# Kernel optimization log

Measured on AMD Instinct MI355X. Metric: run time of the kernel, lower is better.

Reference implementation:

```python
import jax, jax.numpy as jnp
import numpy as np
from jax import lax

GRID_SIZE = 5
SPLINE_ORDER = 3
N_COEF = GRID_SIZE + SPLINE_ORDER  # 8 b-spline basis functions per input
GRID_LO, GRID_HI = -1.0, 1.0


def _grid():
    h = (GRID_HI - GRID_LO) / GRID_SIZE
    return jnp.arange(-SPLINE_ORDER, GRID_SIZE + SPLINE_ORDER + 1, dtype=jnp.float32) * h + GRID_LO


def _bsplines(x):
    # x: [..., in] -> [..., in, N_COEF] via Cox-de Boor recursion (efficient-kan)
    grid = _grid()
    x = x[..., None]
    bases = ((x >= grid[:-1]) & (x < grid[1:])).astype(x.dtype)
    for j in range(1, SPLINE_ORDER + 1):
        bases = ((x - grid[:-(j + 1)]) / (grid[j:-1] - grid[:-(j + 1)]) * bases[..., :-1]
                 + (grid[j + 1:] - x) / (grid[j + 1:] - grid[1:-j]) * bases[..., 1:])
    return bases


def _kan_linear(x, base_w, spline_w):
    # x: [..., in]; base_w: [out, in]; spline_w: [out, in, N_COEF]
    base = jax.nn.silu(x) @ base_w.T
    b = _bsplines(x).reshape(x.shape[:-1] + (-1,))  # [..., in*N_COEF]
    return base + b @ spline_w.reshape(spline_w.shape[0], -1).T


def _kan_conv(x, base_w, spline_w):
    # x: [B, C, H, W]; 3x3 valid KAN convolution
    patches = lax.conv_general_dilated_patches(x, (3, 3), (1, 1), 'VALID')  # [B, C*9, H-2, W-2]
    p = patches.transpose(0, 2, 3, 1)  # [B, Ho, Wo, C*9]
    out = _kan_linear(p, base_w, spline_w)  # [B, Ho, Wo, out]
    return out.transpose(0, 3, 1, 2)


def _maxpool2(x):
    return lax.reduce_window(x, -jnp.inf, lax.max, (1, 1, 2, 2), (1, 1, 2, 2), 'VALID')


def setup_inputs() -> dict:
    key = jax.random.key(0)
    ks = jax.random.split(key, 12)
    B = 2048
    x = jax.random.uniform(ks[0], (B, 1, 28, 28), dtype=jnp.float32)
    s = 0.1
    return {
        'x': x,
        'bw1': jax.random.normal(ks[1], (5, 9), dtype=jnp.float32) * s,
        'sw1': jax.random.normal(ks[2], (5, 9, N_COEF), dtype=jnp.float32) * s,
        'bw2': jax.random.normal(ks[3], (5, 45), dtype=jnp.float32) * s,
        'sw2': jax.random.normal(ks[4], (5, 45, N_COEF), dtype=jnp.float32) * s,
        'bw3': jax.random.normal(ks[5], (2, 45), dtype=jnp.float32) * s,
        'sw3': jax.random.normal(ks[6], (2, 45, N_COEF), dtype=jnp.float32) * s,
        'w1': jax.random.normal(ks[7], (500, 162), dtype=jnp.float32) * 0.05,
        'b1': jnp.zeros((500,), dtype=jnp.float32),
        'w2': jax.random.normal(ks[8], (10, 500), dtype=jnp.float32) * 0.05,
        'b2': jnp.zeros((10,), dtype=jnp.float32),
    }


def reference(x, bw1, sw1, bw2, sw2, bw3, sw3, w1, b1, w2, b2):
    h = _kan_conv(x, bw1, sw1)       # [B, 5, 26, 26]
    h = _maxpool2(h)                 # [B, 5, 13, 13]
    h = _kan_conv(h, bw2, sw2)       # [B, 5, 11, 11]
    h = _kan_conv(h, bw3, sw3)       # [B, 2, 9, 9]
    h = h.reshape(h.shape[0], -1)    # [B, 162]
    h = jax.nn.relu(h @ w1.T + b1)   # [B, 500]
    return h @ w2.T + b2             # [B, 10]
```

## Files before the change

### kernel.cpp

```cpp
#include <hip/hip_runtime.h>


typedef _Float16 h2 __attribute__((ext_vector_type(2)));

__device__ __forceinline__ h2 u2h(unsigned int u) {
  union { unsigned int x; h2 h; } v; v.x = u; return v.h;
}
__device__ __forceinline__ unsigned short f2h_bits(float x) {
  union { _Float16 h; unsigned short u; } v; v.h = (_Float16)x; return v.u;
}
__device__ __forceinline__ unsigned int pack2h(float a, float b) {
  return (unsigned int)f2h_bits(a) | ((unsigned int)f2h_bits(b) << 16);
}
__device__ __forceinline__ float fdot2(h2 a, h2 b, float c) {
  return __builtin_amdgcn_fdot2(a, b, c, false);
}

__device__ __forceinline__ void featurize_regs(float v, uint4& bs, float& silu) {
  silu = v / (1.0f + __expf(-v));
  bs.x = 0u; bs.y = 0u; bs.z = 0u; bs.w = 0u;
  float u = fmaf(v, 2.5f, 5.5f);
  if (u >= 0.0f && u < 11.0f) {
    float tf = floorf(u);
    float f = u - tf, f2 = f * f, f3 = f2 * f, om = 1.0f - f;
    const float c6 = 1.0f / 6.0f;
    float w0 = om * om * om * c6;
    float w1 = (3.0f * f3 - 6.0f * f2 + 4.0f) * c6;
    float w2 = (-3.0f * f3 + 3.0f * f2 + 3.0f * f + 1.0f) * c6;
    float w3 = f3 * c6;
    unsigned long long w01 =
        (unsigned long long)f2h_bits(w0) |
        ((unsigned long long)f2h_bits(w1) << 16) |
        ((unsigned long long)f2h_bits(w2) << 32) |
        ((unsigned long long)f2h_bits(w3) << 48);
    int t = (int)tf;
    int s = 16 * t - 48;
    unsigned long long lo, hi;
    if (s >= 0) {
      lo = (s < 64) ? (w01 << s) : 0ull;
      hi = (s == 0) ? 0ull : ((s < 64) ? (w01 >> (64 - s)) : (w01 << (s - 64)));
    } else {
      lo = w01 >> (-s);
      hi = 0ull;
    }
    bs.x = (unsigned int)lo; bs.y = (unsigned int)(lo >> 32);
    bs.z = (unsigned int)hi; bs.w = (unsigned int)(hi >> 32);
  }
}

__global__ __launch_bounds__(256) void k_prep(
    const float* __restrict__ bw1, const float* __restrict__ sw1,
    const float* __restrict__ bw2, const float* __restrict__ sw2,
    const float* __restrict__ bw3, const float* __restrict__ sw3,
    const float* __restrict__ w1, const float* __restrict__ w2,
    unsigned int* __restrict__ V1s, float* __restrict__ V1b,
    unsigned int* __restrict__ V2s, float* __restrict__ V2b,
    unsigned int* __restrict__ V3s, float* __restrict__ V3b,
    unsigned int* __restrict__ W1p4, float* __restrict__ W2p) {
  int t = blockIdx.x * 256 + threadIdx.x;
  if (t < 180) {
    int p = t & 3, o = (t >> 2) % 5, in = t / 20;
    V1s[t] = pack2h(sw1[(o * 9 + in) * 8 + 2 * p], sw1[(o * 9 + in) * 8 + 2 * p + 1]);
  }
  if (t < 45)  { int o = t % 5, in = t / 5; V1b[t] = bw1[o * 9 + in]; }
  if (t < 900) {
    int p = t & 3, o = (t >> 2) % 5, in = t / 20;
    V2s[t] = pack2h(sw2[(o * 45 + in) * 8 + 2 * p], sw2[(o * 45 + in) * 8 + 2 * p + 1]);
  }
  if (t < 225) { int o = t % 5, in = t / 5; V2b[t] = bw2[o * 45 + in]; }
  if (t < 360) {
    int p = t & 3, o = (t >> 2) & 1, in = t / 8;
    V3s[t] = pack2h(sw3[(o * 45 + in) * 8 + 2 * p], sw3[(o * 45 + in) * 8 + 2 * p + 1]);
  }
  if (t < 90)  { int o = t % 2, in = t / 2; V3b[t] = bw3[o * 45 + in]; }
  if (t < 43008) {
    int j = t & 3, o = (t >> 2) & 511, kpq = t >> 11;
    int kp = kpq * 4 + j;
    W1p4[t] = (o < 500 && kp < 81)
                  ? pack2h(w1[o * 162 + 2 * kp], w1[o * 162 + 2 * kp + 1])
                  : 0u;
  }
  if (t < 5120) {
    int o = t >> 9, k = t & 511;
    W2p[t] = (k < 500) ? w2[o * 500 + k] : 0.0f;
  }
}

__global__ __launch_bounds__(64, 2) void k_fused(
    const float* __restrict__ x,
    const unsigned int* __restrict__ V1s, const float* __restrict__ V1b,
    const unsigned int* __restrict__ V2s, const float* __restrict__ V2b,
    const unsigned int* __restrict__ V3s, const float* __restrict__ V3b,
    const unsigned int* __restrict__ W1p4, const float* __restrict__ W2p,
    const float* __restrict__ b1, const float* __restrict__ b2,
    float* __restrict__ out) {
  __shared__ uint4 bas[845];
  __shared__ float slu[845];
  float*        basF = (float*)bas;
  unsigned int* hpk  = (unsigned int*)slu + 256;
  const int b = blockIdx.x;
  const int lane = threadIdx.x;

  for (int l = lane; l < 784; l += 64) {
    uint4 bs; float sl;
    featurize_regs(x[b * 784 + l], bs, sl);
    bas[l] = bs; slu[l] = sl;
  }

  float h1v[3][5];
  #pragma unroll 1
  for (int it = 0; it < 3; ++it) {
    int p = it * 64 + lane;
    if (p < 169) {
      int py = p / 13, px = p % 13;
      int r0 = py * 2, c0 = px * 2;
      float wacc[4][5];
      #pragma unroll
      for (int wi = 0; wi < 4; ++wi)
        #pragma unroll
        for (int o = 0; o < 5; ++o) wacc[wi][o] = 0.0f;
      #pragma unroll
      for (int r = 0; r < 4; ++r) {
        uint4 q[4]; float sl[4];
        #pragma unroll
        for (int c = 0; c < 4; ++c) {
          q[c]  = bas[(r0 + r) * 28 + c0 + c];
          sl[c] = slu[(r0 + r) * 28 + c0 + c];
        }
        #pragma unroll
        for (int c = 0; c < 4; ++c) {
          h2 a0 = u2h(q[c].x), a1 = u2h(q[c].y), a2 = u2h(q[c].z), a3 = u2h(q[c].w);
          #pragma unroll
          for (int dy = 0; dy < 2; ++dy) {
            #pragma unroll
            for (int dx = 0; dx < 2; ++dx) {
              int ky = r - dy, kx = c - dx;
              if (ky >= 0 && ky < 3 && kx >= 0 && kx < 3) {
                const unsigned int* wp = V1s + (ky * 3 + kx) * 20;
                const float* bp = V1b + (ky * 3 + kx) * 5;
                #pragma unroll
                for (int o = 0; o < 5; ++o) {
                  float acc = wacc[dy * 2 + dx][o];
                  acc = fdot2(a0, u2h(wp[o * 4 + 0]), acc);
                  acc = fdot2(a1, u2h(wp[o * 4 + 1]), acc);
                  acc = fdot2(a2, u2h(wp[o * 4 + 2]), acc);
                  acc = fdot2(a3, u2h(wp[o * 4 + 3]), acc);
                  wacc[dy * 2 + dx][o] = fmaf(sl[c], bp[o], acc);
                }
              }
            }
          }
        }
      }
      #pragma unroll
      for (int o = 0; o < 5; ++o)
        h1v[it][o] = fmaxf(fmaxf(wacc[0][o], wacc[1][o]),
                           fmaxf(wacc[2][o], wacc[3][o]));
    }
  }
  #pragma unroll 1
  for (int it = 0; it < 3; ++it) {
    int p = it * 64 + lane;
    if (p < 169) {
      #pragma unroll
      for (int o = 0; o < 5; ++o) {
        uint4 bs; float sl;
        featurize_regs(h1v[it][o], bs, sl);
        bas[o * 169 + p] = bs; slu[o * 169 + p] = sl;
      }
    }
  }

  float h2v[2][5];
  #pragma unroll 1
  for (int it = 0; it < 2; ++it) {
    int pos = it * 64 + lane;
    if (pos < 121) {
      int y = pos / 11, xx = pos % 11;
      float acc2[5];
      #pragma unroll
      for (int o = 0; o < 5; ++o) acc2[o] = 0.0f;
      #pragma unroll 1
      for (int cky = 0; cky < 15; ++cky) {
        int c = cky / 3, ky = cky % 3;
        int base = c * 169 + (y + ky) * 13 + xx;
        uint4 q0 = bas[base], q1 = bas[base + 1], q2 = bas[base + 2];
        float s0 = slu[base], s1 = slu[base + 1], s2 = slu[base + 2];
        uint4 wq[15]; float wb[15];
        const uint4* wp4 = (const uint4*)(V2s + cky * 60);
        const float* bp  = V2b + cky * 15;
        #pragma unroll
        for (int i = 0; i < 15; ++i) { wq[i] = wp4[i]; wb[i] = bp[i]; }
        #pragma unroll
        for (int kx = 0; kx < 3; ++kx) {
          uint4 q = (kx == 0) ? q0 : ((kx == 1) ? q1 : q2);
          float sl = (kx == 0) ? s0 : ((kx == 1) ? s1 : s2);
          h2 a0 = u2h(q.x), a1 = u2h(q.y), a2 = u2h(q.z), a3 = u2h(q.w);
          #pragma unroll
          for (int o = 0; o < 5; ++o) {
            uint4 w = wq[kx * 5 + o];
            float a = acc2[o];
            a = fdot2(a0, u2h(w.x), a);
            a = fdot2(a1, u2h(w.y), a);
            a = fdot2(a2, u2h(w.z), a);
            a = fdot2(a3, u2h(w.w), a);
            acc2[o] = fmaf(sl, wb[kx * 5 + o], a);
          }
        }
      }
      #pragma unroll
      for (int o = 0; o < 5; ++o) h2v[it][o] = acc2[o];
    }
  }
  #pragma unroll 1
  for (int it = 0; it < 2; ++it) {
    int pos = it * 64 + lane;
    if (pos < 121) {
      #pragma unroll
      for (int o = 0; o < 5; ++o) {
        uint4 bs; float sl;
        featurize_regs(h2v[it][o], bs, sl);
        bas[o * 121 + pos] = bs; slu[o * 121 + pos] = sl;
      }
    }
  }

  float h3v[2][2];
  #pragma unroll 1
  for (int it = 0; it < 2; ++it) {
    int pos = it * 64 + lane;
    if (pos < 81) {
      int y = pos / 9, xx = pos % 9;
      float acc3[2] = {0.f, 0.f};
      #pragma unroll 1
      for (int cky = 0; cky < 15; ++cky) {
        int c = cky / 3, ky = cky % 3;
        int base = c * 121 + (y + ky) * 11 + xx;
        uint4 q0 = bas[base], q1 = bas[base + 1], q2 = bas[base + 2];
        float s0 = slu[base], s1 = slu[base + 1], s2 = slu[base + 2];
        uint4 wq[6]; float wb[6];
        const uint4* wp4 = (const uint4*)(V3s + cky * 24);
        const float* bp  = V3b + cky * 6;
        #pragma unroll
        for (int i = 0; i < 6; ++i) { wq[i] = wp4[i]; wb[i] = bp[i]; }
        #pragma unroll
        for (int kx = 0; kx < 3; ++kx) {
          uint4 q = (kx == 0) ? q0 : ((kx == 1) ? q1 : q2);
          float sl = (kx == 0) ? s0 : ((kx == 1) ? s1 : s2);
          h2 a0 = u2h(q.x), a1 = u2h(q.y), a2 = u2h(q.z), a3 = u2h(q.w);
          #pragma unroll
          for (int o = 0; o < 2; ++o) {
            uint4 w = wq[kx * 2 + o];
            float a = acc3[o];
            a = fdot2(a0, u2h(w.x), a);
            a = fdot2(a1, u2h(w.y), a);
            a = fdot2(a2, u2h(w.z), a);
            a = fdot2(a3, u2h(w.w), a);
            acc3[o] = fmaf(sl, wb[kx * 2 + o], a);
          }
        }
      }
      h3v[it][0] = acc3[0]; h3v[it][1] = acc3[1];
    }
  }
  #pragma unroll 1
  for (int it = 0; it < 2; ++it) {
    int pos = it * 64 + lane;
    if (pos < 81) { slu[pos] = h3v[it][0]; slu[81 + pos] = h3v[it][1]; }
  }
  hpk[lane] = pack2h(slu[2 * lane], slu[2 * lane + 1]);
  {
    int i1 = 64 + lane;
    if (i1 < 84)
      hpk[i1] = (i1 < 81) ? pack2h(slu[2 * i1], slu[2 * i1 + 1]) : 0u;
  }

  float fa[8];
  #pragma unroll
  for (int i = 0; i < 8; ++i) fa[i] = 0.0f;
  {
    const uint4* hp4 = (const uint4*)hpk;
    #pragma unroll 1
    for (int kpq = 0; kpq < 21; ++kpq) {
      uint4 hk = hp4[kpq];
      const uint4* wrow = (const uint4*)W1p4 + kpq * 512 + lane;
      #pragma unroll
      for (int i = 0; i < 8; ++i) {
        uint4 wv = wrow[i * 64];
        float a = fa[i];
        a = fdot2(u2h(hk.x), u2h(wv.x), a);
        a = fdot2(u2h(hk.y), u2h(wv.y), a);
        a = fdot2(u2h(hk.z), u2h(wv.z), a);
        a = fdot2(u2h(hk.w), u2h(wv.w), a);
        fa[i] = a;
      }
    }
  }
  #pragma unroll
  for (int i = 0; i < 8; ++i) {
    int o = lane + 64 * i;
    float bb = (o < 500) ? b1[o] : 0.0f;
    float v = fa[i] + bb;
    basF[o] = (v > 0.0f && o < 500) ? v : 0.0f;
  }

  float hv0, hv1, hv2, hv3, hv4, hv5, hv6, hv7;
  {
    const float4* hf = (const float4*)&basF[lane * 8];
    float4 ha = hf[0], hb = hf[1];
    hv0 = ha.x; hv1 = ha.y; hv2 = ha.z; hv3 = ha.w;
    hv4 = hb.x; hv5 = hb.y; hv6 = hb.z; hv7 = hb.w;
  }
  float acc10[10];
  #pragma unroll
  for (int o = 0; o < 10; ++o) {
    const float4* wp = (const float4*)&W2p[o * 512 + lane * 8];
    float4 w0 = wp[0], w1v = wp[1];
    float s = hv0 * w0.x + hv1 * w0.y + hv2 * w0.z + hv3 * w0.w;
    s += hv4 * w1v.x + hv5 * w1v.y + hv6 * w1v.z + hv7 * w1v.w;
    acc10[o] = s;
  }
  #pragma unroll
  for (int off = 32; off > 0; off >>= 1) {
    #pragma unroll
    for (int o = 0; o < 10; ++o) acc10[o] += __shfl_down(acc10[o], off);
  }
  if (lane == 0) {
    #pragma unroll
    for (int o = 0; o < 10; ++o) out[b * 10 + o] = acc10[o] + b2[o];
  }
}

extern "C" void kernel_launch(void* const* d_in, const int* in_sizes, int n_in,
                              void* d_out, int out_size, void* d_ws, size_t ws_size,
                              hipStream_t stream) {
  (void)in_sizes; (void)n_in; (void)out_size; (void)ws_size;
  const float* x   = (const float*)d_in[0];
  const float* bw1 = (const float*)d_in[1];
  const float* sw1 = (const float*)d_in[2];
  const float* bw2 = (const float*)d_in[3];
  const float* sw2 = (const float*)d_in[4];
  const float* bw3 = (const float*)d_in[5];
  const float* sw3 = (const float*)d_in[6];
  const float* w1  = (const float*)d_in[7];
  const float* b1  = (const float*)d_in[8];
  const float* w2  = (const float*)d_in[9];
  const float* b2  = (const float*)d_in[10];
  float* out = (float*)d_out;

  char* ws = (char*)d_ws;
  unsigned int* V1s  = (unsigned int*)(ws);
  float*        V1b  = (float*)(ws + 768);
  unsigned int* V2s  = (unsigned int*)(ws + 1024);
  float*        V2b  = (float*)(ws + 4672);
  unsigned int* V3s  = (unsigned int*)(ws + 5632);
  float*        V3b  = (float*)(ws + 7168);
  float*        W2p  = (float*)(ws + 7680);
  unsigned int* W1p4 = (unsigned int*)(ws + 28672);

  k_prep<<<168, 256, 0, stream>>>(bw1, sw1, bw2, sw2, bw3, sw3, w1, w2,
                                  V1s, V1b, V2s, V2b, V3s, V3b, W1p4, W2p);
  k_fused<<<2048, 64, 0, stream>>>(x, V1s, V1b, V2s, V2b, V3s, V3b,
                                   W1p4, W2p, b1, b2, out);
}
```

Measured before the change: 136.8 us.

## Double-buffer W1 loads, store silu in fp16, restructure conv1 loop

The FC1 loop now double-buffers the W1 global loads in two register sets, so loads for the next k-group are issued while the current group's dot products run. The silu shared-memory buffer is stored as fp16, which halves its LDS footprint and may allow more blocks per CU, at some precision cost. The conv1 loop nest is reordered and its row loop is no longer unrolled, trading instruction-level parallelism for lower register pressure. The extra wB register set raises VGPR use.

```diff
diff --git a/kernel.cpp b/kernel.cpp
--- a/kernel.cpp
+++ b/kernel.cpp
@@ -8,6 +8,9 @@
 }
 __device__ __forceinline__ unsigned short f2h_bits(float x) {
   union { _Float16 h; unsigned short u; } v; v.h = (_Float16)x; return v.u;
+}
+__device__ __forceinline__ float h2f(unsigned short u) {
+  union { unsigned short u; _Float16 h; } v; v.u = u; return (float)v.h;
 }
 __device__ __forceinline__ unsigned int pack2h(float a, float b) {
   return (unsigned int)f2h_bits(a) | ((unsigned int)f2h_bits(b) << 16);
@@ -74,8 +77,8 @@
   }
   if (t < 90)  { int o = t % 2, in = t / 2; V3b[t] = bw3[o * 45 + in]; }
   if (t < 43008) {
-    int j = t & 3, o = (t >> 2) & 511, kpq = t >> 11;
-    int kp = kpq * 4 + j;
+    int j = t & 3, o = (t >> 2) & 511, g = t >> 11;
+    int kp = g * 4 + j;
     W1p4[t] = (o < 500 && kp < 81)
                   ? pack2h(w1[o * 162 + 2 * kp], w1[o * 162 + 2 * kp + 1])
                   : 0u;
@@ -95,16 +98,18 @@
     const float* __restrict__ b1, const float* __restrict__ b2,
     float* __restrict__ out) {
   __shared__ uint4 bas[845];
-  __shared__ float slu[845];
+  __shared__ unsigned short slu16[848];
   float*        basF = (float*)bas;
-  unsigned int* hpk  = (unsigned int*)slu + 256;
+  float*        h3f  = basF + 2048;
+  unsigned int* hpk  = (unsigned int*)basF + 2560;
   const int b = blockIdx.x;
   const int lane = threadIdx.x;
 
+  #pragma unroll 1
   for (int l = lane; l < 784; l += 64) {
     uint4 bs; float sl;
     featurize_regs(x[b * 784 + l], bs, sl);
-    bas[l] = bs; slu[l] = sl;
+    bas[l] = bs; slu16[l] = f2h_bits(sl);
   }
 
   float h1v[3][5];
@@ -119,33 +124,37 @@
       for (int wi = 0; wi < 4; ++wi)
         #pragma unroll
         for (int o = 0; o < 5; ++o) wacc[wi][o] = 0.0f;
-      #pragma unroll
+      #pragma unroll 1
       for (int r = 0; r < 4; ++r) {
         uint4 q[4]; float sl[4];
         #pragma unroll
         for (int c = 0; c < 4; ++c) {
           q[c]  = bas[(r0 + r) * 28 + c0 + c];
-          sl[c] = slu[(r0 + r) * 28 + c0 + c];
-        }
-        #pragma unroll
-        for (int c = 0; c < 4; ++c) {
-          h2 a0 = u2h(q[c].x), a1 = u2h(q[c].y), a2 = u2h(q[c].z), a3 = u2h(q[c].w);
-          #pragma unroll
-          for (int dy = 0; dy < 2; ++dy) {
+          sl[c] = h2f(slu16[(r0 + r) * 28 + c0 + c]);
+        }
+        #pragma unroll
+        for (int dy = 0; dy < 2; ++dy) {
+          int ky = r - dy;
+          if (ky >= 0 && ky < 3) {
             #pragma unroll
-            for (int dx = 0; dx < 2; ++dx) {
-              int ky = r - dy, kx = c - dx;
-              if (ky >= 0 && ky < 3 && kx >= 0 && kx < 3) {
-                const unsigned int* wp = V1s + (ky * 3 + kx) * 20;
-                const float* bp = V1b + (ky * 3 + kx) * 5;
-                #pragma unroll
-                for (int o = 0; o < 5; ++o) {
-                  float acc = wacc[dy * 2 + dx][o];
-                  acc = fdot2(a0, u2h(wp[o * 4 + 0]), acc);
-                  acc = fdot2(a1, u2h(wp[o * 4 + 1]), acc);
-                  acc = fdot2(a2, u2h(wp[o * 4 + 2]), acc);
-                  acc = fdot2(a3, u2h(wp[o * 4 + 3]), acc);
-                  wacc[dy * 2 + dx][o] = fmaf(sl[c], bp[o], acc);
+            for (int c = 0; c < 4; ++c) {
+              h2 a0 = u2h(q[c].x), a1 = u2h(q[c].y),
+                 a2 = u2h(q[c].z), a3 = u2h(q[c].w);
+              #pragma unroll
+              for (int dx = 0; dx < 2; ++dx) {
+                int kx = c - dx;
+                if (kx >= 0 && kx < 3) {
+                  const unsigned int* wp = V1s + (ky * 3 + kx) * 20;
+                  const float* bp = V1b + (ky * 3 + kx) * 5;
+                  #pragma unroll
+                  for (int o = 0; o < 5; ++o) {
+                    float acc = wacc[dy * 2 + dx][o];
+                    acc = fdot2(a0, u2h(wp[o * 4 + 0]), acc);
+                    acc = fdot2(a1, u2h(wp[o * 4 + 1]), acc);
+                    acc = fdot2(a2, u2h(wp[o * 4 + 2]), acc);
+                    acc = fdot2(a3, u2h(wp[o * 4 + 3]), acc);
+                    wacc[dy * 2 + dx][o] = fmaf(sl[c], bp[o], acc);
+                  }
                 }
               }
             }
@@ -166,7 +175,7 @@
       for (int o = 0; o < 5; ++o) {
         uint4 bs; float sl;
         featurize_regs(h1v[it][o], bs, sl);
-        bas[o * 169 + p] = bs; slu[o * 169 + p] = sl;
+        bas[o * 169 + p] = bs; slu16[o * 169 + p] = f2h_bits(sl);
       }
     }
   }
@@ -182,10 +191,11 @@
       for (int o = 0; o < 5; ++o) acc2[o] = 0.0f;
       #pragma unroll 1
       for (int cky = 0; cky < 15; ++cky) {
-        int c = cky / 3, ky = cky % 3;
+        int c = cky / 3, ky = cky - c * 3;
         int base = c * 169 + (y + ky) * 13 + xx;
         uint4 q0 = bas[base], q1 = bas[base + 1], q2 = bas[base + 2];
-        float s0 = slu[base], s1 = slu[base + 1], s2 = slu[base + 2];
+        float s0 = h2f(slu16[base]), s1 = h2f(slu16[base + 1]),
+              s2 = h2f(slu16[base + 2]);
         uint4 wq[15]; float wb[15];
         const uint4* wp4 = (const uint4*)(V2s + cky * 60);
         const float* bp  = V2b + cky * 15;
@@ -220,7 +230,7 @@
       for (int o = 0; o < 5; ++o) {
         uint4 bs; float sl;
         featurize_regs(h2v[it][o], bs, sl);
-        bas[o * 121 + pos] = bs; slu[o * 121 + pos] = sl;
+        bas[o * 121 + pos] = bs; slu16[o * 121 + pos] = f2h_bits(sl);
       }
     }
   }
@@ -234,10 +244,11 @@
       float acc3[2] = {0.f, 0.f};
       #pragma unroll 1
       for (int cky = 0; cky < 15; ++cky) {
-        int c = cky / 3, ky = cky % 3;
+        int c = cky / 3, ky = cky - c * 3;
         int base = c * 121 + (y + ky) * 11 + xx;
         uint4 q0 = bas[base], q1 = bas[base + 1], q2 = bas[base + 2];
-        float s0 = slu[base], s1 = slu[base + 1], s2 = slu[base + 2];
+        float s0 = h2f(slu16[base]), s1 = h2f(slu16[base + 1]),
+              s2 = h2f(slu16[base + 2]);
         uint4 wq[6]; float wb[6];
         const uint4* wp4 = (const uint4*)(V3s + cky * 24);
         const float* bp  = V3b + cky * 6;
@@ -266,13 +277,13 @@
   #pragma unroll 1
   for (int it = 0; it < 2; ++it) {
     int pos = it * 64 + lane;
-    if (pos < 81) { slu[pos] = h3v[it][0]; slu[81 + pos] = h3v[it][1]; }
-  }
-  hpk[lane] = pack2h(slu[2 * lane], slu[2 * lane + 1]);
+    if (pos < 81) { h3f[pos] = h3v[it][0]; h3f[81 + pos] = h3v[it][1]; }
+  }
+  hpk[lane] = pack2h(h3f[2 * lane], h3f[2 * lane + 1]);
   {
     int i1 = 64 + lane;
     if (i1 < 84)
-      hpk[i1] = (i1 < 81) ? pack2h(slu[2 * i1], slu[2 * i1 + 1]) : 0u;
+      hpk[i1] = (i1 < 81) ? pack2h(h3f[2 * i1], h3f[2 * i1 + 1]) : 0u;
   }
 
   float fa[8];
@@ -280,19 +291,45 @@
   for (int i = 0; i < 8; ++i) fa[i] = 0.0f;
   {
     const uint4* hp4 = (const uint4*)hpk;
+    const uint4* wbase = (const uint4*)W1p4 + lane;
+    uint4 wA[8], wB[8];
+    #pragma unroll
+    for (int i = 0; i < 8; ++i) wA[i] = wbase[i * 64];
     #pragma unroll 1
-    for (int kpq = 0; kpq < 21; ++kpq) {
-      uint4 hk = hp4[kpq];
-      const uint4* wrow = (const uint4*)W1p4 + kpq * 512 + lane;
-      #pragma unroll
-      for (int i = 0; i < 8; ++i) {
-        uint4 wv = wrow[i * 64];
-        float a = fa[i];
-        a = fdot2(u2h(hk.x), u2h(wv.x), a);
-        a = fdot2(u2h(hk.y), u2h(wv.y), a);
-        a = fdot2(u2h(hk.z), u2h(wv.z), a);
-        a = fdot2(u2h(hk.w), u2h(wv.w), a);
-        fa[i] = a;
+    for (int g = 0; g < 21; g += 2) {
+      if (g + 1 < 21) {
+        const uint4* p = wbase + (g + 1) * 512;
+        #pragma unroll
+        for (int i = 0; i < 8; ++i) wB[i] = p[i * 64];
+      }
+      {
+        uint4 hk = hp4[g];
+        #pragma unroll
+        for (int i = 0; i < 8; ++i) {
+          float a = fa[i];
+          a = fdot2(u2h(hk.x), u2h(wA[i].x), a);
+          a = fdot2(u2h(hk.y), u2h(wA[i].y), a);
+          a = fdot2(u2h(hk.z), u2h(wA[i].z), a);
+          a = fdot2(u2h(hk.w), u2h(wA[i].w), a);
+          fa[i] = a;
+        }
+      }
+      if (g + 2 < 21) {
+        const uint4* p = wbase + (g + 2) * 512;
+        #pragma unroll
+        for (int i = 0; i < 8; ++i) wA[i] = p[i * 64];
+      }
+      if (g + 1 < 21) {
+        uint4 hk = hp4[g + 1];
+        #pragma unroll
+        for (int i = 0; i < 8; ++i) {
+          float a = fa[i];
+          a = fdot2(u2h(hk.x), u2h(wB[i].x), a);
+          a = fdot2(u2h(hk.y), u2h(wB[i].y), a);
+          a = fdot2(u2h(hk.z), u2h(wB[i].z), a);
+          a = fdot2(u2h(hk.w), u2h(wB[i].w), a);
+          fa[i] = a;
+        }
       }
     }
   }
```

Measured after the change: 138.1 us. About the same (+0.9%).
